# Optimization experiments

Hardware: AMD Instinct MI355X
Metric: run time of the kernel (lower is better)

The kernel has to match this reference:

```python
import jax, jax.numpy as jnp
import numpy as np

N_QUBITS, Q_DEPTH, N_OUTPUT, BATCH = 8, 6, 8, 16384
_C = np.complex64
_H = (np.array([[1, 1], [1, -1]]) / np.sqrt(2)).astype(_C)
_PX = np.array([[0, 1], [1, 0]], dtype=_C)
_PY = np.array([[0, -1j], [1j, 0]], dtype=_C)
_PZ = np.array([[1, 0], [0, -1]], dtype=_C)

def _swap_rows(n, i, j):
    m = np.eye(n, dtype=_C)
    m[[i, j]] = m[[j, i]]
    return m

_CNOT = _swap_rows(4, 2, 3)          # flip target when control=1
_CZ = np.diag(np.array([1, 1, 1, -1], dtype=_C))
_CSWAP = _swap_rows(8, 5, 6)         # swap |101> <-> |110>
_TOF = _swap_rows(8, 6, 7)           # swap |110> <-> |111>


def _apply(state, U, wires):
    """Apply k-qubit gate U (2^k x 2^k, shared across batch) on given wires.
    state: [B] + [2]*N_QUBITS complex tensor."""
    k = len(wires)
    axes = [w + 1 for w in wires]
    st = jnp.moveaxis(state, axes, list(range(1, k + 1)))
    shp = st.shape
    st = jnp.einsum('ij,bjr->bir', jnp.asarray(U, st.dtype), st.reshape(shp[0], 2 ** k, -1))
    return jnp.moveaxis(st.reshape(shp), list(range(1, k + 1)), axes)


def _apply_batched(state, U, wire):
    """Apply per-sample single-qubit gate U [B,2,2] on `wire`."""
    st = jnp.moveaxis(state, wire + 1, 1)
    shp = st.shape
    st = jnp.einsum('bij,bjr->bir', U, st.reshape(shp[0], 2, -1))
    return jnp.moveaxis(st.reshape(shp), 1, wire + 1)


def _rot_mat(axis, theta):
    """Scalar-angle RX/RY/RZ (axis 0/1/2), PennyLane convention exp(-i theta P / 2)."""
    c = jnp.cos(theta / 2)
    s = jnp.sin(theta / 2)
    z = jnp.zeros_like(c)
    if axis == 0:    # RX
        re = jnp.stack([jnp.stack([c, z]), jnp.stack([z, c])])
        im = jnp.stack([jnp.stack([z, -s]), jnp.stack([-s, z])])
    elif axis == 1:  # RY
        re = jnp.stack([jnp.stack([c, -s]), jnp.stack([s, c])])
        im = jnp.zeros((2, 2), dtype=c.dtype)
    else:            # RZ
        re = jnp.stack([jnp.stack([c, z]), jnp.stack([z, c])])
        im = jnp.stack([jnp.stack([-s, z]), jnp.stack([z, s])])
    return (re.astype(jnp.complex64) + 1j * im.astype(jnp.complex64))


def _ry_batched(theta):
    """Per-sample RY matrices: theta [B] -> [B,2,2] complex64."""
    c = jnp.cos(theta / 2)
    s = jnp.sin(theta / 2)
    U = jnp.stack([jnp.stack([c, -s], -1), jnp.stack([s, c], -1)], -2)
    return U.astype(jnp.complex64)


def _forward(input_features, q_params, d_ry, d_rot, d_g2):
    B = input_features.shape[0]
    n = N_QUBITS
    qw = q_params.reshape(Q_DEPTH, n)
    # |0...0> state, shape [B] + [2]*n
    basis = jnp.zeros((2 ** n,), jnp.complex64).at[0].set(1.0)
    state = (jnp.ones((B, 1), jnp.complex64) * basis[None, :]).reshape((B,) + (2,) * n)
    for w in range(n):
        state = _apply(state, _H, [w])
    two_q = {5: _CNOT, 8: _CZ}
    three_q = {6: _CSWAP, 7: _TOF}
    one_q = {1: _H, 2: _PX, 3: _PY, 4: _PZ}
    for layer in range(Q_DEPTH):
        for node in range(n):
            li, ni = layer % 6, node % 4
            if d_ry[li, ni]:
                state = _apply_batched(state, _ry_batched(input_features[:, node]), node)
            rot = int(d_rot[li, ni])
            if rot < 3:
                state = _apply(state, _rot_mat(rot, qw[layer, node]), [node])
            g2 = int(d_g2[li, ni])
            if g2 in one_q:
                state = _apply(state, one_q[g2], [node])
            elif g2 in two_q:
                state = _apply(state, two_q[g2], [node, (node + 1) % n])
            elif g2 in three_q:
                state = _apply(state, three_q[g2], [node, (node + 1) % n, (node + 2) % n])
    probs = state.real ** 2 + state.imag ** 2  # [B] + [2]*n
    exps = []
    for p in range(N_OUTPUT):
        axes = tuple(i for i in range(1, n + 1) if i != p + 1)
        m = probs.sum(axis=axes)  # [B, 2]
        exps.append(m[:, 0] - m[:, 1])
    return jnp.stack(exps, axis=1)  # [B, N_OUTPUT] float32


def setup_inputs() -> dict:
    key = jax.random.key(0)
    k1, k2, k3, k4, k5 = jax.random.split(key, 5)
    return {
        'input_features': jax.random.normal(k1, (BATCH, N_QUBITS), jnp.float32),
        'q_params': jax.random.normal(k2, (Q_DEPTH * N_QUBITS,), jnp.float32),
        'design_ry': jax.random.randint(k3, (6, 4), 0, 2, jnp.int32),
        'design_rot': jax.random.randint(k4, (6, 4), 0, 4, jnp.int32),
        'design_gate2': jax.random.randint(k5, (6, 4), 0, 9, jnp.int32),
    }


def reference(input_features, q_params, design_ry, design_rot, design_gate2):
    # The circuit design is a static (architecture) choice -> host constants.
    d_ry = np.asarray(design_ry)
    d_rot = np.asarray(design_rot)
    d_g2 = np.asarray(design_gate2)
    return _forward(input_features, q_params, d_ry, d_rot, d_g2)
```

## Files before the change

kernel.cpp:

```cpp
#include <hip/hip_runtime.h>
#include <stdint.h>

#define NQ 8

#define HALF_INV2PI 0.07957747154594767f

typedef float f32x2 __attribute__((ext_vector_type(2)));

__device__ __forceinline__ f32x2 pk2(float x, float y) { f32x2 r; r.x = x; r.y = y; return r; }
__device__ __forceinline__ f32x2 pkb(float x)          { f32x2 r; r.x = x; r.y = x; return r; }

__device__ __forceinline__ f32x2 pk_fma(f32x2 a, f32x2 b, f32x2 c) {
    f32x2 d;
    asm("v_pk_fma_f32 %0, %1, %2, %3" : "=v"(d) : "v"(a), "v"(b), "v"(c));
    return d;
}
__device__ __forceinline__ f32x2 pk_mul(f32x2 a, f32x2 b) {
    f32x2 d;
    asm("v_pk_mul_f32 %0, %1, %2" : "=v"(d) : "v"(a), "v"(b));
    return d;
}
__device__ __forceinline__ f32x2 pk_fma_sa_nh(f32x2 a, f32x2 b, f32x2 c) {
    f32x2 d;
    asm("v_pk_fma_f32 %0, %1, %2, %3 op_sel:[1,0,0] op_sel_hi:[0,1,1] neg_hi:[0,1,0]"
        : "=v"(d) : "v"(a), "v"(b), "v"(c));
    return d;
}
__device__ __forceinline__ f32x2 pk_fma_sa_nl(f32x2 a, f32x2 b, f32x2 c) {
    f32x2 d;
    asm("v_pk_fma_f32 %0, %1, %2, %3 op_sel:[1,0,0] op_sel_hi:[0,1,1] neg_lo:[0,1,0]"
        : "=v"(d) : "v"(a), "v"(b), "v"(c));
    return d;
}
__device__ __forceinline__ f32x2 pk_fma_nh(f32x2 a, f32x2 b, f32x2 c) {
    f32x2 d;
    asm("v_pk_fma_f32 %0, %1, %2, %3 neg_hi:[0,1,0]"
        : "=v"(d) : "v"(a), "v"(b), "v"(c));
    return d;
}

template<int XM>
__device__ __forceinline__ float sx(float v) {
    if constexpr (XM == 0) return v;
    const int x = __float_as_int(v);
    int r;
    if constexpr (XM == 1)      r = __builtin_amdgcn_update_dpp(0, x, 0xB1,  0xF, 0xF, true);
    else if constexpr (XM == 2) r = __builtin_amdgcn_update_dpp(0, x, 0x4E,  0xF, 0xF, true);
    else if constexpr (XM == 8) r = __builtin_amdgcn_update_dpp(0, x, 0x128, 0xF, 0xF, true);
    else                        r = __builtin_amdgcn_ds_swizzle(x, (XM << 10) | 0x1F);
    return __int_as_float(r);
}

template<int XM>
__device__ __forceinline__ f32x2 sxp(f32x2 v) {
    f32x2 r; r.x = sx<XM>(v.x); r.y = sx<XM>(v.y); return r;
}
template<int XM>
__device__ __forceinline__ f32x2 sxp_swap(f32x2 v) {
    f32x2 r; r.x = sx<XM>(v.y); r.y = sx<XM>(v.x); return r;
}

__device__ __forceinline__ void swapv(f32x2& a, f32x2& b) { f32x2 t = a; a = b; b = t; }


template<int Q>
__device__ __forceinline__ void realGate(f32x2 (&v)[8], int laneq,
                                         float a, float b, float d, float e)
{
    if constexpr (Q < 3) {
        constexpr int M = 1 << Q;
        const f32x2 a2 = pkb(a), b2 = pkb(b), d2 = pkb(d), e2 = pkb(e);
#pragma unroll
        for (int i = 0; i < 8; i++) if (!(i & M)) {
            const int j = i | M;
            const f32x2 x0 = v[i], x1 = v[j];
            v[i] = pk_fma(a2, x0, pk_mul(b2, x1));
            v[j] = pk_fma(d2, x0, pk_mul(e2, x1));
        }
    } else {
        constexpr int XM = 1 << (Q - 3);
        const int bit = (laneq >> (Q - 3)) & 1;
        const f32x2 sc2 = pkb(bit ? e : a);
        const f32x2 pc2 = pkb(bit ? d : b);
#pragma unroll
        for (int i = 0; i < 8; i++) {
            const f32x2 p = sxp<XM>(v[i]);
            v[i] = pk_fma(sc2, v[i], pk_mul(pc2, p));
        }
    }
}

template<int Q>
__device__ __forceinline__ void applyRX(f32x2 (&v)[8], int laneq, float c, float s)
{
    const f32x2 cc = pkb(c), ss = pkb(s);
    if constexpr (Q < 3) {
        constexpr int M = 1 << Q;
#pragma unroll
        for (int i = 0; i < 8; i++) if (!(i & M)) {
            const int j = i | M;
            const f32x2 x0 = v[i], x1 = v[j];
            v[i] = pk_fma_sa_nh(x1, ss, pk_mul(cc, x0));
            v[j] = pk_fma_sa_nh(x0, ss, pk_mul(cc, x1));
        }
    } else {
        constexpr int XM = 1 << (Q - 3);
#pragma unroll
        for (int i = 0; i < 8; i++) {
            const f32x2 ps = sxp_swap<XM>(v[i]);
            v[i] = pk_fma_nh(ps, ss, pk_mul(cc, v[i]));
        }
    }
}

template<int Q>
__device__ __forceinline__ void applyRZ(f32x2 (&v)[8], int laneq, float c, float s)
{
    const f32x2 cc = pkb(c);
    if constexpr (Q >= 3) {
        const int bit = (laneq >> (Q - 3)) & 1;
        const float t = bit ? -s : s;
        const f32x2 tt = pkb(t);
#pragma unroll
        for (int i = 0; i < 8; i++)
            v[i] = pk_fma_sa_nh(v[i], tt, pk_mul(cc, v[i]));
    } else {
        const f32x2 ss = pkb(s);
#pragma unroll
        for (int i = 0; i < 8; i++) {
            if ((i >> Q) & 1) v[i] = pk_fma_sa_nl(v[i], ss, pk_mul(cc, v[i]));
            else              v[i] = pk_fma_sa_nh(v[i], ss, pk_mul(cc, v[i]));
        }
    }
}

template<int Q>
__device__ __forceinline__ void applyZ(f32x2 (&v)[8], int laneq)
{
    if constexpr (Q >= 3) {
        const bool f = ((laneq >> (Q - 3)) & 1) != 0;
#pragma unroll
        for (int i = 0; i < 8; i++) {
            v[i].x = f ? -v[i].x : v[i].x;
            v[i].y = f ? -v[i].y : v[i].y;
        }
    } else {
#pragma unroll
        for (int i = 0; i < 8; i++) if ((i >> Q) & 1) {
            v[i].x = -v[i].x; v[i].y = -v[i].y;
        }
    }
}

template<int Q>
__device__ __forceinline__ void applyX(f32x2 (&v)[8], int laneq)
{
    if constexpr (Q < 3) {
        constexpr int M = 1 << Q;
#pragma unroll
        for (int i = 0; i < 8; i++) if (!(i & M)) {
            swapv(v[i], v[i | M]);
        }
    } else {
        constexpr int XM = 1 << (Q - 3);
#pragma unroll
        for (int i = 0; i < 8; i++) {
            v[i] = sxp<XM>(v[i]);
        }
    }
}

template<int Q>
__device__ __forceinline__ void applyY(f32x2 (&v)[8], int laneq)
{
    if constexpr (Q < 3) {
        constexpr int M = 1 << Q;
#pragma unroll
        for (int i = 0; i < 8; i++) if (!(i & M)) {
            const int j = i | M;
            const f32x2 x0 = v[i], x1 = v[j];
            v[i] = pk2(x1.y, -x1.x);
            v[j] = pk2(-x0.y, x0.x);
        }
    } else {
        constexpr int XM = 1 << (Q - 3);
        const int bit = (laneq >> (Q - 3)) & 1;
#pragma unroll
        for (int i = 0; i < 8; i++) {
            const f32x2 p = sxp<XM>(v[i]);
            v[i].x = bit ? -p.y : p.y;
            v[i].y = bit ? p.x : -p.x;
        }
    }
}

template<int C, int T>
__device__ __forceinline__ void applyCZ(f32x2 (&v)[8], int laneq)
{
#pragma unroll
    for (int i = 0; i < 8; i++) {
        const int g = i | (laneq << 3);
        const bool f = (((g >> C) & (g >> T)) & 1) != 0;
        v[i].x = f ? -v[i].x : v[i].x;
        v[i].y = f ? -v[i].y : v[i].y;
    }
}

template<int CM, int M>
__device__ __forceinline__ void applyCPerm(f32x2 (&v)[8], int laneq)
{
    constexpr int LX  = M >> 3;
    constexpr int PL  = M & 7;
    constexpr int CML = CM & 7;
    constexpr int CMH = CM >> 3;
    if constexpr (LX != 0) {
#pragma unroll
        for (int i = 0; i < 8; i++) {
            if ((i & CML) == CML) {
                const f32x2 p = sxp<LX>(v[i]);
                if constexpr (CMH != 0) {
                    const bool c = (laneq & CMH) == CMH;
                    v[i].x = c ? p.x : v[i].x;
                    v[i].y = c ? p.y : v[i].y;
                } else {
                    v[i] = p;
                }
            }
        }
    } else {
#pragma unroll
        for (int i = 0; i < 8; i++) {
            if (!(i & PL) && ((i & CML) == CML)) {
                const int j = i | PL;
                if constexpr (CMH != 0) {
                    const bool c = (laneq & CMH) == CMH;
                    const f32x2 t0 = v[i];
                    v[i].x = c ? v[j].x : v[i].x;  v[i].y = c ? v[j].y : v[i].y;
                    v[j].x = c ? t0.x : v[j].x;    v[j].y = c ? t0.y : v[j].y;
                } else {
                    swapv(v[i], v[j]);
                }
            }
        }
    }
}

template<int C, int T1, int T2>
__device__ __forceinline__ void applyCSWAP(f32x2 (&v)[8], int laneq)
{
    constexpr int M  = (1 << T1) | (1 << T2);
    constexpr int LX = M >> 3;
    constexpr int PL = M & 7;

    if constexpr (LX == 0) {
#pragma unroll
        for (int i = 0; i < 8; i++) {
            if (((i >> T1) & 1) && !((i >> T2) & 1)) {
                bool skip = false;
                if constexpr (C < 3) { if (!((i >> C) & 1)) skip = true; }
                if (!skip) {
                    const int j = i ^ PL;
                    if constexpr (C >= 3) {
                        const bool c = ((laneq >> (C - 3)) & 1) != 0;
                        const f32x2 t0 = v[i];
                        v[i].x = c ? v[j].x : v[i].x;  v[i].y = c ? v[j].y : v[i].y;
                        v[j].x = c ? t0.x : v[j].x;    v[j].y = c ? t0.y : v[j].y;
                    } else {
                        swapv(v[i], v[j]);
                    }
                }
            }
        }
    } else if constexpr (PL == 0) {
        bool c = ((((laneq >> (T1 - 3)) ^ (laneq >> (T2 - 3))) & 1) != 0);
        if constexpr (C >= 3) c = c && (((laneq >> (C - 3)) & 1) != 0);
#pragma unroll
        for (int i = 0; i < 8; i++) {
            bool skip = false;
            if constexpr (C < 3) { if (!((i >> C) & 1)) skip = true; }
            if (!skip) {
                const f32x2 p = sxp<LX>(v[i]);
                v[i].x = c ? p.x : v[i].x;
                v[i].y = c ? p.y : v[i].y;
            }
        }
    } else {
        constexpr int TL = (PL == (1 << T1)) ? T2 : T1;
        const bool laneT = ((laneq >> (TL - 3)) & 1) != 0;
        bool cc = true;
        if constexpr (C >= 3) cc = ((laneq >> (C - 3)) & 1) != 0;
#pragma unroll
        for (int i = 0; i < 8; i++) {
            if (!(i & PL)) {
                bool skip = false;
                if constexpr (C < 3) { if (!((i >> C) & 1)) skip = true; }
                if (!skip) {
                    const int j = i | PL;
                    const f32x2 a = sxp<LX>(v[j]);
                    const f32x2 b = sxp<LX>(v[i]);
                    const bool ci = cc && laneT;
                    const bool cj = cc && !laneT;
                    v[i].x = ci ? a.x : v[i].x;  v[i].y = ci ? a.y : v[i].y;
                    v[j].x = cj ? b.x : v[j].x;  v[j].y = cj ? b.y : v[j].y;
                }
            }
        }
    }
}

template<int N>
__device__ __forceinline__ void nodeStep(f32x2 (&v)[8], int laneq,
                                         const float2* ryCS, const float2* rotCS,
                                         int layer, int dryL, int drotL, int dg2L)
{
    constexpr int N1 = (N + 1) & 7;
    constexpr int N2 = (N + 2) & 7;
    constexpr int SL = N & 3;

    const bool ryOn = ((dryL >> SL) & 1) != 0;
    const int rot = (drotL >> (2 * SL)) & 3;

    if (rot < 3) {
        const float2 t = rotCS[layer * NQ + N];
        const float cb = t.x, sb = t.y;
        if (ryOn && rot == 1) {
            const float2 a = ryCS[N];
            const float c = cb * a.x - sb * a.y;
            const float s = sb * a.x + cb * a.y;
            realGate<N>(v, laneq, c, -s, s, c);
        } else {
            if (ryOn) {
                const float2 a = ryCS[N];
                realGate<N>(v, laneq, a.x, -a.y, a.y, a.x);
            }
            if (rot == 0)      applyRX<N>(v, laneq, cb, sb);
            else if (rot == 1) realGate<N>(v, laneq, cb, -sb, sb, cb);
            else               applyRZ<N>(v, laneq, cb, sb);
        }
    } else if (ryOn) {
        const float2 a = ryCS[N];
        realGate<N>(v, laneq, a.x, -a.y, a.y, a.x);
    }

    const int g2 = (dg2L >> (4 * SL)) & 15;
    switch (g2) {
        case 1: {
            const float r = 0.70710678118654752f;
            realGate<N>(v, laneq, r, r, r, -r);
        } break;
        case 2: applyX<N>(v, laneq); break;
        case 3: applyY<N>(v, laneq); break;
        case 4: applyZ<N>(v, laneq); break;
        case 5: applyCPerm<(1 << N), (1 << N1)>(v, laneq); break;
        case 6: applyCSWAP<N, N1, N2>(v, laneq); break;
        case 7: applyCPerm<(1 << N) | (1 << N1), (1 << N2)>(v, laneq); break;
        case 8: applyCZ<N, N1>(v, laneq); break;
        default: break;
    }
}

__global__ __launch_bounds__(256, 4) void qsim_kernel(
    const float* __restrict__ feats,
    const float* __restrict__ qp,
    const int* __restrict__ dry,
    const int* __restrict__ drot,
    const int* __restrict__ dg2,
    float* __restrict__ out,
    int B)
{
    __shared__ float2 lds_ry[8][8];
    __shared__ float2 lds_rot[48];

    const int tid   = threadIdx.x;
    const int laneq = tid & 31;
    const int grp   = tid >> 5;
    const int b     = blockIdx.x * 8 + grp;

    if (tid < 48) {
        const float th = qp[tid] * HALF_INV2PI;
        lds_rot[tid] = make_float2(__builtin_amdgcn_cosf(th), __builtin_amdgcn_sinf(th));
    }
    if (laneq < 8) {
        const float th = feats[(size_t)b * NQ + laneq] * HALF_INV2PI;
        lds_ry[grp][laneq] = make_float2(__builtin_amdgcn_cosf(th), __builtin_amdgcn_sinf(th));
    }

    uint32_t dryP = 0;
    uint64_t drotP = 0;
    uint32_t g2P0 = 0, g2P1 = 0, g2P2 = 0;
#pragma unroll
    for (int q = 0; q < 6; q++) {
        const int4 a = ((const int4*)dry)[q];
        dryP |= (uint32_t)(__builtin_amdgcn_readfirstlane(a.x) & 1) << (4 * q + 0);
        dryP |= (uint32_t)(__builtin_amdgcn_readfirstlane(a.y) & 1) << (4 * q + 1);
        dryP |= (uint32_t)(__builtin_amdgcn_readfirstlane(a.z) & 1) << (4 * q + 2);
        dryP |= (uint32_t)(__builtin_amdgcn_readfirstlane(a.w) & 1) << (4 * q + 3);
        const int4 r = ((const int4*)drot)[q];
        drotP |= (uint64_t)(__builtin_amdgcn_readfirstlane(r.x) & 3) << (8 * q + 0);
        drotP |= (uint64_t)(__builtin_amdgcn_readfirstlane(r.y) & 3) << (8 * q + 2);
        drotP |= (uint64_t)(__builtin_amdgcn_readfirstlane(r.z) & 3) << (8 * q + 4);
        drotP |= (uint64_t)(__builtin_amdgcn_readfirstlane(r.w) & 3) << (8 * q + 6);
        const int4 g = ((const int4*)dg2)[q];
        const uint32_t gg = ((uint32_t)(__builtin_amdgcn_readfirstlane(g.x) & 15))
                          | ((uint32_t)(__builtin_amdgcn_readfirstlane(g.y) & 15) << 4)
                          | ((uint32_t)(__builtin_amdgcn_readfirstlane(g.z) & 15) << 8)
                          | ((uint32_t)(__builtin_amdgcn_readfirstlane(g.w) & 15) << 12);
        if      (q == 0) g2P0 |= gg;
        else if (q == 1) g2P0 |= gg << 16;
        else if (q == 2) g2P1 |= gg;
        else if (q == 3) g2P1 |= gg << 16;
        else if (q == 4) g2P2 |= gg;
        else             g2P2 |= gg << 16;
    }

    __syncthreads();

    const float2* ryCS  = &lds_ry[grp][0];
    const float2* rotCS = &lds_rot[0];

    f32x2 v[8];
#pragma unroll
    for (int i = 0; i < 8; i++) { v[i] = pk2(0.0625f, 0.0f); }

#pragma unroll 1
    for (int layer = 0; layer < 6; layer++) {
        const int dryL  = (int)((dryP >> (layer * 4)) & 0xF);
        const int drotL = (int)((drotP >> (layer * 8)) & 0xFF);
        const uint32_t g2w = (layer >= 4) ? g2P2 : ((layer >= 2) ? g2P1 : g2P0);
        const int dg2L  = (int)((g2w >> ((layer & 1) * 16)) & 0xFFFF);

        nodeStep<0>(v, laneq, ryCS, rotCS, layer, dryL, drotL, dg2L);
        nodeStep<1>(v, laneq, ryCS, rotCS, layer, dryL, drotL, dg2L);
        nodeStep<2>(v, laneq, ryCS, rotCS, layer, dryL, drotL, dg2L);
        nodeStep<3>(v, laneq, ryCS, rotCS, layer, dryL, drotL, dg2L);
        nodeStep<4>(v, laneq, ryCS, rotCS, layer, dryL, drotL, dg2L);
        nodeStep<5>(v, laneq, ryCS, rotCS, layer, dryL, drotL, dg2L);
        nodeStep<6>(v, laneq, ryCS, rotCS, layer, dryL, drotL, dg2L);
        nodeStep<7>(v, laneq, ryCS, rotCS, layer, dryL, drotL, dg2L);
    }

    float tot = 0.f, s0 = 0.f, s1 = 0.f, s2 = 0.f;
#pragma unroll
    for (int i = 0; i < 8; i++) {
        const float p = v[i].x * v[i].x + v[i].y * v[i].y;
        tot += p;
        if (!(i & 1)) s0 += p;
        if (!(i & 2)) s1 += p;
        if (!(i & 4)) s2 += p;
    }
    float e[3] = { 2.f * s0 - tot, 2.f * s1 - tot, 2.f * s2 - tot };

#pragma unroll
    for (int q = 0; q < 3; q++) {
        e[q] += sx<1>(e[q]);
        e[q] += sx<2>(e[q]);
        e[q] += sx<4>(e[q]);
        e[q] += sx<8>(e[q]);
        e[q] += sx<16>(e[q]);
    }
    { float pv = sx<1>(tot);  tot = (laneq & 1)  ? (pv - tot) : (pv + tot); }
    { float pv = sx<2>(tot);  tot = (laneq & 2)  ? (pv - tot) : (pv + tot); }
    { float pv = sx<4>(tot);  tot = (laneq & 4)  ? (pv - tot) : (pv + tot); }
    { float pv = sx<8>(tot);  tot = (laneq & 8)  ? (pv - tot) : (pv + tot); }
    { float pv = sx<16>(tot); tot = (laneq & 16) ? (pv - tot) : (pv + tot); }

    float* ob = out + (size_t)b * NQ;
    if (laneq == 0) { ob[0] = e[0]; ob[1] = e[1]; ob[2] = e[2]; }
    if (laneq && !(laneq & (laneq - 1)))
        ob[3 + __builtin_ctz(laneq)] = tot;
}

extern "C" void kernel_launch(void* const* d_in, const int* in_sizes, int n_in,
                              void* d_out, int out_size, void* d_ws, size_t ws_size,
                              hipStream_t stream)
{
    (void)n_in; (void)out_size; (void)d_ws; (void)ws_size;
    const float* feats   = (const float*)d_in[0];
    const float* qparams = (const float*)d_in[1];
    const int* dry       = (const int*)d_in[2];
    const int* drot      = (const int*)d_in[3];
    const int* dg2       = (const int*)d_in[4];
    float* out           = (float*)d_out;

    const int B = in_sizes[0] / NQ;
    const int blocks = (B + 7) / 8;
    qsim_kernel<<<blocks, 256, 0, stream>>>(feats, qparams, dry, drot, dg2, out, B);
}
```

Baseline: 107.2 us.

## Process two batch samples per 32-lane group with 16 amplitudes per lane

Each 32-lane group now simulates two samples at once, so each lane holds 16 amplitudes instead of 8, and blocks cover 16 samples. The per-layer design decoding, branching and shared rotation coefficients are amortised over two states, and lane swizzles carry more independent work, which gives more instruction-level parallelism. In exchange register pressure doubles, which may reduce occupancy, and the grid halves to 1024 blocks.

```diff
diff --git a/kernel.cpp b/kernel.cpp
--- a/kernel.cpp
+++ b/kernel.cpp
@@ -64,14 +64,14 @@
 
 
 template<int Q>
-__device__ __forceinline__ void realGate(f32x2 (&v)[8], int laneq,
+__device__ __forceinline__ void realGate(f32x2 (&v)[16], int laneq,
                                          float a, float b, float d, float e)
 {
     if constexpr (Q < 3) {
         constexpr int M = 1 << Q;
         const f32x2 a2 = pkb(a), b2 = pkb(b), d2 = pkb(d), e2 = pkb(e);
 #pragma unroll
-        for (int i = 0; i < 8; i++) if (!(i & M)) {
+        for (int i = 0; i < 16; i++) if (!(i & M)) {
             const int j = i | M;
             const f32x2 x0 = v[i], x1 = v[j];
             v[i] = pk_fma(a2, x0, pk_mul(b2, x1));
@@ -83,7 +83,7 @@
         const f32x2 sc2 = pkb(bit ? e : a);
         const f32x2 pc2 = pkb(bit ? d : b);
 #pragma unroll
-        for (int i = 0; i < 8; i++) {
+        for (int i = 0; i < 16; i++) {
             const f32x2 p = sxp<XM>(v[i]);
             v[i] = pk_fma(sc2, v[i], pk_mul(pc2, p));
         }
@@ -91,13 +91,44 @@
 }
 
 template<int Q>
-__device__ __forceinline__ void applyRX(f32x2 (&v)[8], int laneq, float c, float s)
+__device__ __forceinline__ void realGateD(f32x2 (&v)[16], int laneq,
+                                          float a0, float b0, float d0, float e0,
+                                          float a1, float b1, float d1, float e1)
+{
+    if constexpr (Q < 3) {
+        constexpr int M = 1 << Q;
+        const f32x2 a2[2] = { pkb(a0), pkb(a1) }, b2[2] = { pkb(b0), pkb(b1) };
+        const f32x2 d2[2] = { pkb(d0), pkb(d1) }, e2[2] = { pkb(e0), pkb(e1) };
+#pragma unroll
+        for (int i = 0; i < 16; i++) if (!(i & M)) {
+            const int j = i | M;
+            const int el = i >> 3;
+            const f32x2 x0 = v[i], x1 = v[j];
+            v[i] = pk_fma(a2[el], x0, pk_mul(b2[el], x1));
+            v[j] = pk_fma(d2[el], x0, pk_mul(e2[el], x1));
+        }
+    } else {
+        constexpr int XM = 1 << (Q - 3);
+        const int bit = (laneq >> (Q - 3)) & 1;
+        const f32x2 sc2[2] = { pkb(bit ? e0 : a0), pkb(bit ? e1 : a1) };
+        const f32x2 pc2[2] = { pkb(bit ? d0 : b0), pkb(bit ? d1 : b1) };
+#pragma unroll
+        for (int i = 0; i < 16; i++) {
+            const int el = i >> 3;
+            const f32x2 p = sxp<XM>(v[i]);
+            v[i] = pk_fma(sc2[el], v[i], pk_mul(pc2[el], p));
+        }
+    }
+}
+
+template<int Q>
+__device__ __forceinline__ void applyRX(f32x2 (&v)[16], int laneq, float c, float s)
 {
     const f32x2 cc = pkb(c), ss = pkb(s);
     if constexpr (Q < 3) {
         constexpr int M = 1 << Q;
 #pragma unroll
-        for (int i = 0; i < 8; i++) if (!(i & M)) {
+        for (int i = 0; i < 16; i++) if (!(i & M)) {
             const int j = i | M;
             const f32x2 x0 = v[i], x1 = v[j];
             v[i] = pk_fma_sa_nh(x1, ss, pk_mul(cc, x0));
@@ -106,7 +137,7 @@
     } else {
         constexpr int XM = 1 << (Q - 3);
 #pragma unroll
-        for (int i = 0; i < 8; i++) {
+        for (int i = 0; i < 16; i++) {
             const f32x2 ps = sxp_swap<XM>(v[i]);
             v[i] = pk_fma_nh(ps, ss, pk_mul(cc, v[i]));
         }
@@ -114,7 +145,7 @@
 }
 
 template<int Q>
-__device__ __forceinline__ void applyRZ(f32x2 (&v)[8], int laneq, float c, float s)
+__device__ __forceinline__ void applyRZ(f32x2 (&v)[16], int laneq, float c, float s)
 {
     const f32x2 cc = pkb(c);
     if constexpr (Q >= 3) {
@@ -122,61 +153,61 @@
         const float t = bit ? -s : s;
         const f32x2 tt = pkb(t);
 #pragma unroll
-        for (int i = 0; i < 8; i++)
+        for (int i = 0; i < 16; i++)
             v[i] = pk_fma_sa_nh(v[i], tt, pk_mul(cc, v[i]));
     } else {
         const f32x2 ss = pkb(s);
 #pragma unroll
-        for (int i = 0; i < 8; i++) {
-            if ((i >> Q) & 1) v[i] = pk_fma_sa_nl(v[i], ss, pk_mul(cc, v[i]));
-            else              v[i] = pk_fma_sa_nh(v[i], ss, pk_mul(cc, v[i]));
-        }
-    }
-}
-
-template<int Q>
-__device__ __forceinline__ void applyZ(f32x2 (&v)[8], int laneq)
+        for (int i = 0; i < 16; i++) {
+            if (((i & 7) >> Q) & 1) v[i] = pk_fma_sa_nl(v[i], ss, pk_mul(cc, v[i]));
+            else                    v[i] = pk_fma_sa_nh(v[i], ss, pk_mul(cc, v[i]));
+        }
+    }
+}
+
+template<int Q>
+__device__ __forceinline__ void applyZ(f32x2 (&v)[16], int laneq)
 {
     if constexpr (Q >= 3) {
         const bool f = ((laneq >> (Q - 3)) & 1) != 0;
 #pragma unroll
-        for (int i = 0; i < 8; i++) {
+        for (int i = 0; i < 16; i++) {
             v[i].x = f ? -v[i].x : v[i].x;
             v[i].y = f ? -v[i].y : v[i].y;
         }
     } else {
 #pragma unroll
-        for (int i = 0; i < 8; i++) if ((i >> Q) & 1) {
+        for (int i = 0; i < 16; i++) if (((i & 7) >> Q) & 1) {
             v[i].x = -v[i].x; v[i].y = -v[i].y;
         }
     }
 }
 
 template<int Q>
-__device__ __forceinline__ void applyX(f32x2 (&v)[8], int laneq)
+__device__ __forceinline__ void applyX(f32x2 (&v)[16], int laneq)
 {
     if constexpr (Q < 3) {
         constexpr int M = 1 << Q;
 #pragma unroll
-        for (int i = 0; i < 8; i++) if (!(i & M)) {
+        for (int i = 0; i < 16; i++) if (!(i & M)) {
             swapv(v[i], v[i | M]);
         }
     } else {
         constexpr int XM = 1 << (Q - 3);
 #pragma unroll
-        for (int i = 0; i < 8; i++) {
+        for (int i = 0; i < 16; i++) {
             v[i] = sxp<XM>(v[i]);
         }
     }
 }
 
 template<int Q>
-__device__ __forceinline__ void applyY(f32x2 (&v)[8], int laneq)
+__device__ __forceinline__ void applyY(f32x2 (&v)[16], int laneq)
 {
     if constexpr (Q < 3) {
         constexpr int M = 1 << Q;
 #pragma unroll
-        for (int i = 0; i < 8; i++) if (!(i & M)) {
+        for (int i = 0; i < 16; i++) if (!(i & M)) {
             const int j = i | M;
             const f32x2 x0 = v[i], x1 = v[j];
             v[i] = pk2(x1.y, -x1.x);
@@ -186,7 +217,7 @@
         constexpr int XM = 1 << (Q - 3);
         const int bit = (laneq >> (Q - 3)) & 1;
 #pragma unroll
-        for (int i = 0; i < 8; i++) {
+        for (int i = 0; i < 16; i++) {
             const f32x2 p = sxp<XM>(v[i]);
             v[i].x = bit ? -p.y : p.y;
             v[i].y = bit ? p.x : -p.x;
@@ -195,11 +226,11 @@
 }
 
 template<int C, int T>
-__device__ __forceinline__ void applyCZ(f32x2 (&v)[8], int laneq)
-{
-#pragma unroll
-    for (int i = 0; i < 8; i++) {
-        const int g = i | (laneq << 3);
+__device__ __forceinline__ void applyCZ(f32x2 (&v)[16], int laneq)
+{
+#pragma unroll
+    for (int i = 0; i < 16; i++) {
+        const int g = (i & 7) | (laneq << 3);
         const bool f = (((g >> C) & (g >> T)) & 1) != 0;
         v[i].x = f ? -v[i].x : v[i].x;
         v[i].y = f ? -v[i].y : v[i].y;
@@ -207,7 +238,7 @@
 }
 
 template<int CM, int M>
-__device__ __forceinline__ void applyCPerm(f32x2 (&v)[8], int laneq)
+__device__ __forceinline__ void applyCPerm(f32x2 (&v)[16], int laneq)
 {
     constexpr int LX  = M >> 3;
     constexpr int PL  = M & 7;
@@ -215,8 +246,8 @@
     constexpr int CMH = CM >> 3;
     if constexpr (LX != 0) {
 #pragma unroll
-        for (int i = 0; i < 8; i++) {
-            if ((i & CML) == CML) {
+        for (int i = 0; i < 16; i++) {
+            if (((i & 7) & CML) == CML) {
                 const f32x2 p = sxp<LX>(v[i]);
                 if constexpr (CMH != 0) {
                     const bool c = (laneq & CMH) == CMH;
@@ -229,8 +260,8 @@
         }
     } else {
 #pragma unroll
-        for (int i = 0; i < 8; i++) {
-            if (!(i & PL) && ((i & CML) == CML)) {
+        for (int i = 0; i < 16; i++) {
+            if (!(i & PL) && (((i & 7) & CML) == CML)) {
                 const int j = i | PL;
                 if constexpr (CMH != 0) {
                     const bool c = (laneq & CMH) == CMH;
@@ -246,7 +277,7 @@
 }
 
 template<int C, int T1, int T2>
-__device__ __forceinline__ void applyCSWAP(f32x2 (&v)[8], int laneq)
+__device__ __forceinline__ void applyCSWAP(f32x2 (&v)[16], int laneq)
 {
     constexpr int M  = (1 << T1) | (1 << T2);
     constexpr int LX = M >> 3;
@@ -254,10 +285,11 @@
 
     if constexpr (LX == 0) {
 #pragma unroll
-        for (int i = 0; i < 8; i++) {
-            if (((i >> T1) & 1) && !((i >> T2) & 1)) {
+        for (int i = 0; i < 16; i++) {
+            const int k = i & 7;
+            if (((k >> T1) & 1) && !((k >> T2) & 1)) {
                 bool skip = false;
-                if constexpr (C < 3) { if (!((i >> C) & 1)) skip = true; }
+                if constexpr (C < 3) { if (!((k >> C) & 1)) skip = true; }
                 if (!skip) {
                     const int j = i ^ PL;
                     if constexpr (C >= 3) {
@@ -275,9 +307,9 @@
         bool c = ((((laneq >> (T1 - 3)) ^ (laneq >> (T2 - 3))) & 1) != 0);
         if constexpr (C >= 3) c = c && (((laneq >> (C - 3)) & 1) != 0);
 #pragma unroll
-        for (int i = 0; i < 8; i++) {
+        for (int i = 0; i < 16; i++) {
             bool skip = false;
-            if constexpr (C < 3) { if (!((i >> C) & 1)) skip = true; }
+            if constexpr (C < 3) { if (!(((i & 7) >> C) & 1)) skip = true; }
             if (!skip) {
                 const f32x2 p = sxp<LX>(v[i]);
                 v[i].x = c ? p.x : v[i].x;
@@ -290,10 +322,10 @@
         bool cc = true;
         if constexpr (C >= 3) cc = ((laneq >> (C - 3)) & 1) != 0;
 #pragma unroll
-        for (int i = 0; i < 8; i++) {
+        for (int i = 0; i < 16; i++) {
             if (!(i & PL)) {
                 bool skip = false;
-                if constexpr (C < 3) { if (!((i >> C) & 1)) skip = true; }
+                if constexpr (C < 3) { if (!(((i & 7) >> C) & 1)) skip = true; }
                 if (!skip) {
                     const int j = i | PL;
                     const f32x2 a = sxp<LX>(v[j]);
@@ -309,8 +341,9 @@
 }
 
 template<int N>
-__device__ __forceinline__ void nodeStep(f32x2 (&v)[8], int laneq,
-                                         const float2* ryCS, const float2* rotCS,
+__device__ __forceinline__ void nodeStep(f32x2 (&v)[16], int laneq,
+                                         const float2* ry0, const float2* ry1,
+                                         const float2* rotCS,
                                          int layer, int dryL, int drotL, int dg2L)
 {
     constexpr int N1 = (N + 1) & 7;
@@ -324,22 +357,24 @@
         const float2 t = rotCS[layer * NQ + N];
         const float cb = t.x, sb = t.y;
         if (ryOn && rot == 1) {
-            const float2 a = ryCS[N];
-            const float c = cb * a.x - sb * a.y;
-            const float s = sb * a.x + cb * a.y;
-            realGate<N>(v, laneq, c, -s, s, c);
+            const float2 A0 = ry0[N], A1 = ry1[N];
+            const float c0 = cb * A0.x - sb * A0.y, s0 = sb * A0.x + cb * A0.y;
+            const float c1 = cb * A1.x - sb * A1.y, s1 = sb * A1.x + cb * A1.y;
+            realGateD<N>(v, laneq, c0, -s0, s0, c0, c1, -s1, s1, c1);
         } else {
             if (ryOn) {
-                const float2 a = ryCS[N];
-                realGate<N>(v, laneq, a.x, -a.y, a.y, a.x);
+                const float2 A0 = ry0[N], A1 = ry1[N];
+                realGateD<N>(v, laneq, A0.x, -A0.y, A0.y, A0.x,
+                                        A1.x, -A1.y, A1.y, A1.x);
             }
             if (rot == 0)      applyRX<N>(v, laneq, cb, sb);
             else if (rot == 1) realGate<N>(v, laneq, cb, -sb, sb, cb);
             else               applyRZ<N>(v, laneq, cb, sb);
         }
     } else if (ryOn) {
-        const float2 a = ryCS[N];
-        realGate<N>(v, laneq, a.x, -a.y, a.y, a.x);
+        const float2 A0 = ry0[N], A1 = ry1[N];
+        realGateD<N>(v, laneq, A0.x, -A0.y, A0.y, A0.x,
+                                A1.x, -A1.y, A1.y, A1.x);
     }
 
     const int g2 = (dg2L >> (4 * SL)) & 15;
@@ -368,21 +403,24 @@
     float* __restrict__ out,
     int B)
 {
-    __shared__ float2 lds_ry[8][8];
+    __shared__ float2 lds_ry[16][8];
     __shared__ float2 lds_rot[48];
 
     const int tid   = threadIdx.x;
     const int laneq = tid & 31;
     const int grp   = tid >> 5;
-    const int b     = blockIdx.x * 8 + grp;
+    const int b0    = blockIdx.x * 16 + grp * 2;
 
     if (tid < 48) {
         const float th = qp[tid] * HALF_INV2PI;
         lds_rot[tid] = make_float2(__builtin_amdgcn_cosf(th), __builtin_amdgcn_sinf(th));
     }
-    if (laneq < 8) {
-        const float th = feats[(size_t)b * NQ + laneq] * HALF_INV2PI;
-        lds_ry[grp][laneq] = make_float2(__builtin_amdgcn_cosf(th), __builtin_amdgcn_sinf(th));
+    if (laneq < 16) {
+        const int e = laneq >> 3;
+        const int n = laneq & 7;
+        const float th = feats[(size_t)(b0 + e) * NQ + n] * HALF_INV2PI;
+        lds_ry[grp * 2 + e][n] = make_float2(__builtin_amdgcn_cosf(th),
+                                             __builtin_amdgcn_sinf(th));
     }
 
     uint32_t dryP = 0;
@@ -415,12 +453,13 @@
 
     __syncthreads();
 
-    const float2* ryCS  = &lds_ry[grp][0];
+    const float2* ry0   = &lds_ry[grp * 2 + 0][0];
+    const float2* ry1   = &lds_ry[grp * 2 + 1][0];
     const float2* rotCS = &lds_rot[0];
 
-    f32x2 v[8];
-#pragma unroll
-    for (int i = 0; i < 8; i++) { v[i] = pk2(0.0625f, 0.0f); }
+    f32x2 v[16];
+#pragma unroll
+    for (int i = 0; i < 16; i++) { v[i] = pk2(0.0625f, 0.0f); }
 
 #pragma unroll 1
     for (int layer = 0; layer < 6; layer++) {
@@ -429,45 +468,49 @@
         const uint32_t g2w = (layer >= 4) ? g2P2 : ((layer >= 2) ? g2P1 : g2P0);
         const int dg2L  = (int)((g2w >> ((layer & 1) * 16)) & 0xFFFF);
 
-        nodeStep<0>(v, laneq, ryCS, rotCS, layer, dryL, drotL, dg2L);
-        nodeStep<1>(v, laneq, ryCS, rotCS, layer, dryL, drotL, dg2L);
-        nodeStep<2>(v, laneq, ryCS, rotCS, layer, dryL, drotL, dg2L);
-        nodeStep<3>(v, laneq, ryCS, rotCS, layer, dryL, drotL, dg2L);
-        nodeStep<4>(v, laneq, ryCS, rotCS, layer, dryL, drotL, dg2L);
-        nodeStep<5>(v, laneq, ryCS, rotCS, layer, dryL, drotL, dg2L);
-        nodeStep<6>(v, laneq, ryCS, rotCS, layer, dryL, drotL, dg2L);
-        nodeStep<7>(v, laneq, ryCS, rotCS, layer, dryL, drotL, dg2L);
-    }
-
-    float tot = 0.f, s0 = 0.f, s1 = 0.f, s2 = 0.f;
-#pragma unroll
-    for (int i = 0; i < 8; i++) {
-        const float p = v[i].x * v[i].x + v[i].y * v[i].y;
-        tot += p;
-        if (!(i & 1)) s0 += p;
-        if (!(i & 2)) s1 += p;
-        if (!(i & 4)) s2 += p;
-    }
-    float e[3] = { 2.f * s0 - tot, 2.f * s1 - tot, 2.f * s2 - tot };
-
-#pragma unroll
-    for (int q = 0; q < 3; q++) {
-        e[q] += sx<1>(e[q]);
-        e[q] += sx<2>(e[q]);
-        e[q] += sx<4>(e[q]);
-        e[q] += sx<8>(e[q]);
-        e[q] += sx<16>(e[q]);
-    }
-    { float pv = sx<1>(tot);  tot = (laneq & 1)  ? (pv - tot) : (pv + tot); }
-    { float pv = sx<2>(tot);  tot = (laneq & 2)  ? (pv - tot) : (pv + tot); }
-    { float pv = sx<4>(tot);  tot = (laneq & 4)  ? (pv - tot) : (pv + tot); }
-    { float pv = sx<8>(tot);  tot = (laneq & 8)  ? (pv - tot) : (pv + tot); }
-    { float pv = sx<16>(tot); tot = (laneq & 16) ? (pv - tot) : (pv + tot); }
-
-    float* ob = out + (size_t)b * NQ;
-    if (laneq == 0) { ob[0] = e[0]; ob[1] = e[1]; ob[2] = e[2]; }
-    if (laneq && !(laneq & (laneq - 1)))
-        ob[3 + __builtin_ctz(laneq)] = tot;
+        nodeStep<0>(v, laneq, ry0, ry1, rotCS, layer, dryL, drotL, dg2L);
+        nodeStep<1>(v, laneq, ry0, ry1, rotCS, layer, dryL, drotL, dg2L);
+        nodeStep<2>(v, laneq, ry0, ry1, rotCS, layer, dryL, drotL, dg2L);
+        nodeStep<3>(v, laneq, ry0, ry1, rotCS, layer, dryL, drotL, dg2L);
+        nodeStep<4>(v, laneq, ry0, ry1, rotCS, layer, dryL, drotL, dg2L);
+        nodeStep<5>(v, laneq, ry0, ry1, rotCS, layer, dryL, drotL, dg2L);
+        nodeStep<6>(v, laneq, ry0, ry1, rotCS, layer, dryL, drotL, dg2L);
+        nodeStep<7>(v, laneq, ry0, ry1, rotCS, layer, dryL, drotL, dg2L);
+    }
+
+#pragma unroll
+    for (int el = 0; el < 2; el++) {
+        float tot = 0.f, s0 = 0.f, s1 = 0.f, s2 = 0.f;
+#pragma unroll
+        for (int k = 0; k < 8; k++) {
+            const int i = el * 8 + k;
+            const float p = v[i].x * v[i].x + v[i].y * v[i].y;
+            tot += p;
+            if (!(k & 1)) s0 += p;
+            if (!(k & 2)) s1 += p;
+            if (!(k & 4)) s2 += p;
+        }
+        float e[3] = { 2.f * s0 - tot, 2.f * s1 - tot, 2.f * s2 - tot };
+
+#pragma unroll
+        for (int q = 0; q < 3; q++) {
+            e[q] += sx<1>(e[q]);
+            e[q] += sx<2>(e[q]);
+            e[q] += sx<4>(e[q]);
+            e[q] += sx<8>(e[q]);
+            e[q] += sx<16>(e[q]);
+        }
+        { float pv = sx<1>(tot);  tot = (laneq & 1)  ? (pv - tot) : (pv + tot); }
+        { float pv = sx<2>(tot);  tot = (laneq & 2)  ? (pv - tot) : (pv + tot); }
+        { float pv = sx<4>(tot);  tot = (laneq & 4)  ? (pv - tot) : (pv + tot); }
+        { float pv = sx<8>(tot);  tot = (laneq & 8)  ? (pv - tot) : (pv + tot); }
+        { float pv = sx<16>(tot); tot = (laneq & 16) ? (pv - tot) : (pv + tot); }
+
+        float* ob = out + (size_t)(b0 + el) * NQ;
+        if (laneq == 0) { ob[0] = e[0]; ob[1] = e[1]; ob[2] = e[2]; }
+        if (laneq && !(laneq & (laneq - 1)))
+            ob[3 + __builtin_ctz(laneq)] = tot;
+    }
 }
 
 extern "C" void kernel_launch(void* const* d_in, const int* in_sizes, int n_in,
@@ -483,6 +526,6 @@
     float* out           = (float*)d_out;
 
     const int B = in_sizes[0] / NQ;
-    const int blocks = (B + 7) / 8;
+    const int blocks = (B + 15) / 16;
     qsim_kernel<<<blocks, 256, 0, stream>>>(feats, qparams, dry, drot, dg2, out, B);
 }
```

Result: slower. 115.4 us (+7.6%).
